# Kernel tuning notes

Hardware: AMD Instinct MI355X
Metric: run time of the kernel (lower is better)

The kernel has to match this reference:

```python
import jax, jax.numpy as jnp
import numpy as np

E, T, D, H = 8, 16384, 2048, 1024  # experts, routed tokens, hidden_size, moe_intermediate_size


def setup_inputs() -> dict:
    key = jax.random.key(0)
    k1, k2, k3, k4 = jax.random.split(key, 4)
    x = jax.random.normal(k1, (T, D), jnp.float32)
    # scale params like a trained init
    w1 = jax.random.normal(k2, (E, H, D), jnp.float32) * 0.02
    w2 = jax.random.normal(k3, (E, D, H), jnp.float32) * 0.02
    w3 = jax.random.normal(k4, (E, H, D), jnp.float32) * 0.02
    # uneven per-expert token counts summing exactly to T (tokens pre-sorted by expert)
    num_tokens_per_expert = jnp.array([3000, 1000, 2500, 1500, 2000, 2200, 1800, 2384], jnp.int32)
    return {"x": x, "w1": w1, "w2": w2, "w3": w3,
            "num_tokens_per_expert": num_tokens_per_expert}


def reference(x, w1, w2, w3, num_tokens_per_expert):
    # Grouped (ragged) GEMM expert FFN: for tokens of expert e,
    #   out = (gelu_tanh(x @ w1[e].T) * (x @ w3[e].T)) @ w2[e].T
    counts = num_tokens_per_expert.astype(jnp.int32)
    wt = lambda w: jnp.swapaxes(w, -1, -2)  # [E, in, out]
    h = jax.nn.gelu(jax.lax.ragged_dot(x, wt(w1), counts), approximate=True)  # [T, H]
    h = h * jax.lax.ragged_dot(x, wt(w3), counts)                             # [T, H]
    out = jax.lax.ragged_dot(h, wt(w2), counts)                               # [T, D]
    return out
```

## Files before the change

kernel.cpp:

```cpp
#include <hip/hip_runtime.h>
#include <hip/hip_bf16.h>
#include <math.h>

constexpr int T_ = 16384;
constexpr int D_ = 2048;
constexpr int H_ = 1024;
constexpr int E_ = 8;

constexpr int BM = 128, BK = 64;
constexpr int MT128 = T_ / 128 + E_;
constexpr int NT16  = 16;
constexpr int NGEMM = MT128 * NT16;

typedef __bf16 bf16x8 __attribute__((ext_vector_type(8)));
typedef float  f32x4  __attribute__((ext_vector_type(4)));

__device__ __forceinline__ int imin(int a, int b) { return a < b ? a : b; }

__device__ __forceinline__ bf16x8 cvt8(const float* p) {
    float4 u = *reinterpret_cast<const float4*>(p);
    float4 v = *reinterpret_cast<const float4*>(p + 4);
    bf16x8 r;
    r[0] = (__bf16)u.x; r[1] = (__bf16)u.y; r[2] = (__bf16)u.z; r[3] = (__bf16)u.w;
    r[4] = (__bf16)v.x; r[5] = (__bf16)v.y; r[6] = (__bf16)v.z; r[7] = (__bf16)v.w;
    return r;
}

__device__ __forceinline__ bf16x8 ld_lds8(const char* lds, int row, int kbyte) {
    int byte = row * 128 + (kbyte ^ ((row & 7) << 4));
    return *reinterpret_cast<const bf16x8*>(lds + byte);
}

template<int K_>
__device__ __forceinline__ void stage_glds(char* lds, const __bf16* __restrict__ src,
                                           int valid, int tid) {
    int wave = tid >> 6, l = tid & 63;
#pragma unroll
    for (int i = 0; i < 4; ++i) {
        int chunk = wave * 4 + i;
        int row = chunk * 8 + (l >> 3);
        int rc = imin(row, valid - 1);
        int colb = ((l & 7) * 16) ^ ((row & 7) << 4);
        const char* gp = reinterpret_cast<const char*>(src)
                       + (size_t)rc * (K_ * 2) + colb;
        __builtin_amdgcn_global_load_lds(
            (const __attribute__((address_space(1))) void*)gp,
            (__attribute__((address_space(3))) void*)(lds + chunk * 1024), 16, 0, 0);
    }
}

__device__ __forceinline__ bool find_expert(const int* __restrict__ counts, int mt,
                                            int& e, int& row0, int& valid) {
    int macc = 0, start = 0;
    e = -1;
    for (int i = 0; i < E_; ++i) {
        int c = counts[i];
        int t = (c + BM - 1) >> 7;
        if (e < 0 && mt < macc + t) {
            int lm = mt - macc;
            e = i; row0 = start + lm * BM; valid = imin(BM, c - lm * BM);
        }
        macc += t; start += c;
    }
    return e >= 0;
}

template<int K_, bool FUSE>
__global__ __launch_bounds__(256, 4) void gemm128(
        const __bf16* __restrict__ A, const __bf16* __restrict__ Bw,
        const int* __restrict__ counts,
        __bf16* __restrict__ hout, float* __restrict__ fout,
        const float* __restrict__ cvt_src, __bf16* __restrict__ cvt_dst,
        int cvt_n8, int nGemm) {
    if ((int)blockIdx.x >= nGemm) {
        int nb = (int)gridDim.x - nGemm;
        int i = ((int)blockIdx.x - nGemm) * 256 + (int)threadIdx.x;
        int stride = nb * 256;
        for (; i < cvt_n8; i += stride)
            *reinterpret_cast<bf16x8*>(cvt_dst + (size_t)i * 8) = cvt8(cvt_src + (size_t)i * 8);
        return;
    }
    __shared__ alignas(16) char sA[128 * 128];
    __shared__ alignas(16) char sB[128 * 128];

    int tid = threadIdx.x;
    int f = (int)blockIdx.x;
    int swz = (f & 7) * (NGEMM / 8) + (f >> 3);
    int nt = swz % NT16, mt = swz / NT16;

    int e, row0, valid;
    if (!find_expert(counts, mt, e, row0, valid)) return;

    int wid = tid >> 6, lane = tid & 63;
    int wr = wid >> 1, wc = wid & 1;
    int frow = lane & 15, fkb = (lane >> 4) * 16;

    const __bf16* Ab = A  + (size_t)row0 * K_;
    const __bf16* Bb = Bw + (size_t)e * 2048 * K_ + (size_t)(nt * 128) * K_;

    f32x4 acc[4][4] = {};

    for (int k0 = 0; k0 < K_; k0 += BK) {
        stage_glds<K_>(sA, Ab + k0, valid, tid);
        stage_glds<K_>(sB, Bb + k0, 128, tid);
        __syncthreads();
#pragma unroll
        for (int kk = 0; kk < BK; kk += 32) {
            int kb = kk * 2 + fkb;
            bf16x8 a[4], b[4];
#pragma unroll
            for (int m = 0; m < 4; ++m) a[m] = ld_lds8(sA, wr * 64 + m * 16 + frow, kb);
#pragma unroll
            for (int n = 0; n < 4; ++n) b[n] = ld_lds8(sB, wc * 64 + n * 16 + frow, kb);
#pragma unroll
            for (int m = 0; m < 4; ++m)
#pragma unroll
                for (int n = 0; n < 4; ++n)
                    acc[m][n] = __builtin_amdgcn_mfma_f32_16x16x32_bf16(a[m], b[n], acc[m][n], 0, 0, 0);
        }
        __syncthreads();
    }

    int q = lane >> 4;
#pragma unroll
    for (int m = 0; m < 4; ++m)
#pragma unroll
        for (int j = 0; j < 4; ++j) {
            int lrow = wr * 64 + m * 16 + q * 4 + j;
            if (lrow < valid) {
                size_t rg = (size_t)(row0 + lrow);
                if (FUSE) {
#pragma unroll
                    for (int p = 0; p < 2; ++p) {
                        float c1 = acc[m][2 * p][j], c3 = acc[m][2 * p + 1][j];
                        float inner = 0.7978845608028654f * (c1 + 0.044715f * c1 * c1 * c1);
                        float g = 0.5f * c1 * (1.0f + tanhf(inner));
                        int col = nt * 64 + wc * 32 + p * 16 + frow;
                        hout[rg * H_ + col] = (__bf16)(g * c3);
                    }
                } else {
#pragma unroll
                    for (int n = 0; n < 4; ++n) {
                        int col = nt * 128 + wc * 64 + n * 16 + frow;
                        fout[rg * D_ + col] = acc[m][n][j];
                    }
                }
            }
        }
}

__global__ __launch_bounds__(256) void prep(const float* __restrict__ x,
                                            __bf16* __restrict__ xb,
                                            const float* __restrict__ w1,
                                            const float* __restrict__ w3,
                                            __bf16* __restrict__ wb) {
    int bid = blockIdx.x;
    if (bid < 2048) {
        int n8 = T_ * D_ / 8;
        int i = bid * 256 + threadIdx.x, stride = 2048 * 256;
        for (; i < n8; i += stride)
            *reinterpret_cast<bf16x8*>(xb + (size_t)i * 8) = cvt8(x + (size_t)i * 8);
    } else {
        int R = (bid - 2048) & 2047, e = (bid - 2048) >> 11;
        int g = R >> 5, r5 = R & 31;
        const float* src = (r5 < 16 ? w1 : w3)
                         + ((size_t)e * H_ + g * 16 + (r5 & 15)) * D_;
        __bf16* dst = wb + ((size_t)e * 2048 + R) * D_;
        int d = threadIdx.x * 8;
        *reinterpret_cast<bf16x8*>(dst + d) = cvt8(src + d);
    }
}

extern "C" void kernel_launch(void* const* d_in, const int* in_sizes, int n_in,
                              void* d_out, int out_size, void* d_ws, size_t ws_size,
                              hipStream_t stream) {
    const float* x      = (const float*)d_in[0];
    const float* w1     = (const float*)d_in[1];
    const float* w2     = (const float*)d_in[2];
    const float* w3     = (const float*)d_in[3];
    const int*   counts = (const int*)d_in[4];
    float* out = (float*)d_out;

    const size_t XB  = (size_t)T_ * D_ * 2;
    const size_t HB  = (size_t)T_ * H_ * 2;
    const size_t WIB = (size_t)E_ * 2 * H_ * D_ * 2;

    char* ws = (char*)d_ws;
    __bf16* xb   = (__bf16*)(ws);
    __bf16* hbuf = (__bf16*)(ws + XB);
    __bf16* wb   = (__bf16*)(ws + XB + HB);
    __bf16* w2b  = (__bf16*)(ws + XB + HB + WIB);
    (void)ws_size;

    prep<<<2048 + E_ * 2048, 256, 0, stream>>>(x, xb, w1, w3, wb);

    gemm128<D_, true ><<<NGEMM + 512, 256, 0, stream>>>(
        xb, wb, counts, hbuf, nullptr, w2, w2b, E_ * D_ * H_ / 8, NGEMM);

    gemm128<H_, false><<<NGEMM, 256, 0, stream>>>(
        hbuf, w2b, counts, nullptr, out, nullptr, nullptr, 0, NGEMM);
}
```

Measured before the change: 328.7 us.

## Double-buffer LDS tiles with async global_load_lds prefetch and MFMA priority

Turns the single-buffered K loop into a double-buffered pipeline. The next K tile is issued via global_load_lds into the alternate LDS buffer before computing the current one, with explicit vmcnt waits and raw s_barriers in place of __syncthreads. It also raises wave priority around the MFMA block and lowers launch bounds to 2 blocks per CU, since LDS use per block doubles to 64KB. The aim is to hide global load latency behind matrix math, at the cost of lower occupancy.

```diff
diff --git a/kernel.cpp b/kernel.cpp
--- a/kernel.cpp
+++ b/kernel.cpp
@@ -16,6 +16,9 @@
 typedef float  f32x4  __attribute__((ext_vector_type(4)));
 
 __device__ __forceinline__ int imin(int a, int b) { return a < b ? a : b; }
+
+#define SCHED0 __builtin_amdgcn_sched_barrier(0)
+#define BARX do { SCHED0; __builtin_amdgcn_s_barrier(); SCHED0; } while (0)
 
 __device__ __forceinline__ bf16x8 cvt8(const float* p) {
     float4 u = *reinterpret_cast<const float4*>(p);
@@ -66,7 +69,7 @@
 }
 
 template<int K_, bool FUSE>
-__global__ __launch_bounds__(256, 4) void gemm128(
+__global__ __launch_bounds__(256, 2) void gemm128db(
         const __bf16* __restrict__ A, const __bf16* __restrict__ Bw,
         const int* __restrict__ counts,
         __bf16* __restrict__ hout, float* __restrict__ fout,
@@ -80,8 +83,9 @@
             *reinterpret_cast<bf16x8*>(cvt_dst + (size_t)i * 8) = cvt8(cvt_src + (size_t)i * 8);
         return;
     }
-    __shared__ alignas(16) char sA[128 * 128];
-    __shared__ alignas(16) char sB[128 * 128];
+    constexpr int NT = K_ / BK;
+    __shared__ alignas(16) char sA[2][128 * 128];
+    __shared__ alignas(16) char sB[2][128 * 128];
 
     int tid = threadIdx.x;
     int f = (int)blockIdx.x;
@@ -100,25 +104,39 @@
 
     f32x4 acc[4][4] = {};
 
-    for (int k0 = 0; k0 < K_; k0 += BK) {
-        stage_glds<K_>(sA, Ab + k0, valid, tid);
-        stage_glds<K_>(sB, Bb + k0, 128, tid);
-        __syncthreads();
+    stage_glds<K_>(sA[0], Ab, valid, tid);
+    stage_glds<K_>(sB[0], Bb, 128, tid);
+
+    for (int t = 0; t < NT; ++t) {
+        int c = t & 1, nc = c ^ 1;
+        if (t + 1 < NT) {
+            stage_glds<K_>(sA[nc], Ab + (t + 1) * BK, valid, tid);
+            stage_glds<K_>(sB[nc], Bb + (t + 1) * BK, 128, tid);
+            asm volatile("s_waitcnt vmcnt(8)" ::: "memory");
+        } else {
+            asm volatile("s_waitcnt vmcnt(0)" ::: "memory");
+        }
+        SCHED0;
+        BARX;
 #pragma unroll
         for (int kk = 0; kk < BK; kk += 32) {
             int kb = kk * 2 + fkb;
             bf16x8 a[4], b[4];
 #pragma unroll
-            for (int m = 0; m < 4; ++m) a[m] = ld_lds8(sA, wr * 64 + m * 16 + frow, kb);
-#pragma unroll
-            for (int n = 0; n < 4; ++n) b[n] = ld_lds8(sB, wc * 64 + n * 16 + frow, kb);
+            for (int m = 0; m < 4; ++m) a[m] = ld_lds8(sA[c], wr * 64 + m * 16 + frow, kb);
+#pragma unroll
+            for (int n = 0; n < 4; ++n) b[n] = ld_lds8(sB[c], wc * 64 + n * 16 + frow, kb);
+            asm volatile("s_waitcnt lgkmcnt(0)" ::: "memory");
+            SCHED0;
+            __builtin_amdgcn_s_setprio(1);
 #pragma unroll
             for (int m = 0; m < 4; ++m)
 #pragma unroll
                 for (int n = 0; n < 4; ++n)
                     acc[m][n] = __builtin_amdgcn_mfma_f32_16x16x32_bf16(a[m], b[n], acc[m][n], 0, 0, 0);
-        }
-        __syncthreads();
+            __builtin_amdgcn_s_setprio(0);
+        }
+        BARX;
     }
 
     int q = lane >> 4;
@@ -194,9 +212,9 @@
 
     prep<<<2048 + E_ * 2048, 256, 0, stream>>>(x, xb, w1, w3, wb);
 
-    gemm128<D_, true ><<<NGEMM + 512, 256, 0, stream>>>(
+    gemm128db<D_, true ><<<NGEMM + 512, 256, 0, stream>>>(
         xb, wb, counts, hbuf, nullptr, w2, w2b, E_ * D_ * H_ / 8, NGEMM);
 
-    gemm128<H_, false><<<NGEMM, 256, 0, stream>>>(
+    gemm128db<H_, false><<<NGEMM, 256, 0, stream>>>(
         hbuf, w2b, counts, nullptr, out, nullptr, nullptr, 0, NGEMM);
 }
```

Result: slower. 430.3 us (+30.9%).

## Fuse both expert GEMMs into one persistent kernel with per-tile dependency counters

Applied to the files above, without the earlier changes.

Replaces the two GEMM launches with a single persistent kernel of 768 blocks. Each block walks a task list: w2 conversion tasks first, then the up-projection tiles, then the down-projection tiles. Down-projection tiles spin on atomic counters until w2 is converted and all 16 up-projection tiles of their row block are done. This removes the kernel boundary and lets the second GEMM overlap the tail of the first, at the cost of spin-wait overhead, an extra memset, and deadlock risk if not every block is resident at once. The path is only taken when the workspace has room for the counters; otherwise the old two-launch path runs.

```diff
diff --git a/kernel.cpp b/kernel.cpp
--- a/kernel.cpp
+++ b/kernel.cpp
@@ -11,6 +11,10 @@
 constexpr int MT128 = T_ / 128 + E_;
 constexpr int NT16  = 16;
 constexpr int NGEMM = MT128 * NT16;
+
+constexpr int NW2   = 512;
+constexpr int NTASK = NW2 + 2 * NGEMM;
+constexpr int PERS  = 768;
 
 typedef __bf16 bf16x8 __attribute__((ext_vector_type(8)));
 typedef float  f32x4  __attribute__((ext_vector_type(4)));
@@ -63,6 +67,120 @@
         macc += t; start += c;
     }
     return e >= 0;
+}
+
+template<int K_, bool FUSE>
+__device__ __forceinline__ void gemm_body(char* sA, char* sB, int tid,
+        int nt, int e, int row0, int valid,
+        const __bf16* __restrict__ A, const __bf16* __restrict__ Bw,
+        __bf16* __restrict__ hout, float* __restrict__ fout) {
+    int wid = tid >> 6, lane = tid & 63;
+    int wr = wid >> 1, wc = wid & 1;
+    int frow = lane & 15, fkb = (lane >> 4) * 16;
+
+    const __bf16* Ab = A  + (size_t)row0 * K_;
+    const __bf16* Bb = Bw + (size_t)e * 2048 * K_ + (size_t)(nt * 128) * K_;
+
+    f32x4 acc[4][4] = {};
+
+    for (int k0 = 0; k0 < K_; k0 += BK) {
+        stage_glds<K_>(sA, Ab + k0, valid, tid);
+        stage_glds<K_>(sB, Bb + k0, 128, tid);
+        __syncthreads();
+#pragma unroll
+        for (int kk = 0; kk < BK; kk += 32) {
+            int kb = kk * 2 + fkb;
+            bf16x8 a[4], b[4];
+#pragma unroll
+            for (int m = 0; m < 4; ++m) a[m] = ld_lds8(sA, wr * 64 + m * 16 + frow, kb);
+#pragma unroll
+            for (int n = 0; n < 4; ++n) b[n] = ld_lds8(sB, wc * 64 + n * 16 + frow, kb);
+#pragma unroll
+            for (int m = 0; m < 4; ++m)
+#pragma unroll
+                for (int n = 0; n < 4; ++n)
+                    acc[m][n] = __builtin_amdgcn_mfma_f32_16x16x32_bf16(a[m], b[n], acc[m][n], 0, 0, 0);
+        }
+        __syncthreads();
+    }
+
+    int q = lane >> 4;
+#pragma unroll
+    for (int m = 0; m < 4; ++m)
+#pragma unroll
+        for (int j = 0; j < 4; ++j) {
+            int lrow = wr * 64 + m * 16 + q * 4 + j;
+            if (lrow < valid) {
+                size_t rg = (size_t)(row0 + lrow);
+                if (FUSE) {
+#pragma unroll
+                    for (int p = 0; p < 2; ++p) {
+                        float c1 = acc[m][2 * p][j], c3 = acc[m][2 * p + 1][j];
+                        float inner = 0.7978845608028654f * (c1 + 0.044715f * c1 * c1 * c1);
+                        float g = 0.5f * c1 * (1.0f + tanhf(inner));
+                        int col = nt * 64 + wc * 32 + p * 16 + frow;
+                        hout[rg * H_ + col] = (__bf16)(g * c3);
+                    }
+                } else {
+#pragma unroll
+                    for (int n = 0; n < 4; ++n) {
+                        int col = nt * 128 + wc * 64 + n * 16 + frow;
+                        fout[rg * D_ + col] = acc[m][n][j];
+                    }
+                }
+            }
+        }
+}
+
+__global__ __launch_bounds__(256, 4) void ffn_fused(
+        const __bf16* __restrict__ xb, const __bf16* __restrict__ wb,
+        __bf16* __restrict__ w2b, const float* __restrict__ w2,
+        const int* __restrict__ counts,
+        __bf16* __restrict__ hbuf, float* __restrict__ out,
+        int* __restrict__ ctr) {
+    __shared__ alignas(16) char sA[128 * 128];
+    __shared__ alignas(16) char sB[128 * 128];
+    int tid = threadIdx.x;
+
+    for (int task = (int)blockIdx.x; task < NTASK; task += PERS) {
+        if (task < NW2) {
+            int n8 = E_ * D_ * H_ / 8;
+            for (int i = task * 256 + tid; i < n8; i += NW2 * 256)
+                *reinterpret_cast<bf16x8*>(w2b + (size_t)i * 8) = cvt8(w2 + (size_t)i * 8);
+            __threadfence();
+            __syncthreads();
+            if (tid == 0) atomicAdd(&ctr[1], 1);
+            __syncthreads();
+        } else if (task < NW2 + NGEMM) {
+            int f = task - NW2;
+            int swz = (f & 7) * (NGEMM / 8) + (f >> 3);
+            int nt = swz % NT16, mt = swz / NT16;
+            int e, row0, valid;
+            bool ok = find_expert(counts, mt, e, row0, valid);
+            if (ok) {
+                gemm_body<D_, true>(sA, sB, tid, nt, e, row0, valid, xb, wb, hbuf, nullptr);
+                __threadfence();
+            }
+            __syncthreads();
+            if (ok && tid == 0) atomicAdd(&ctr[2 + mt], 1);
+            __syncthreads();
+        } else {
+            int f = task - NW2 - NGEMM;
+            int swz = (f & 7) * (NGEMM / 8) + (f >> 3);
+            int nt = swz % NT16, mt = swz / NT16;
+            int e, row0, valid;
+            if (find_expert(counts, mt, e, row0, valid)) {
+                if (tid == 0) {
+                    while (atomicAdd(&ctr[1], 0) < NW2) __builtin_amdgcn_s_sleep(32);
+                    while (atomicAdd(&ctr[2 + mt], 0) < NT16) __builtin_amdgcn_s_sleep(32);
+                    __threadfence();
+                }
+                __syncthreads();
+                gemm_body<H_, false>(sA, sB, tid, nt, e, row0, valid, hbuf, w2b, nullptr, out);
+                __syncthreads();
+            }
+        }
+    }
 }
 
 template<int K_, bool FUSE>
@@ -82,71 +200,13 @@
     }
     __shared__ alignas(16) char sA[128 * 128];
     __shared__ alignas(16) char sB[128 * 128];
-
     int tid = threadIdx.x;
     int f = (int)blockIdx.x;
     int swz = (f & 7) * (NGEMM / 8) + (f >> 3);
     int nt = swz % NT16, mt = swz / NT16;
-
     int e, row0, valid;
     if (!find_expert(counts, mt, e, row0, valid)) return;
-
-    int wid = tid >> 6, lane = tid & 63;
-    int wr = wid >> 1, wc = wid & 1;
-    int frow = lane & 15, fkb = (lane >> 4) * 16;
-
-    const __bf16* Ab = A  + (size_t)row0 * K_;
-    const __bf16* Bb = Bw + (size_t)e * 2048 * K_ + (size_t)(nt * 128) * K_;
-
-    f32x4 acc[4][4] = {};
-
-    for (int k0 = 0; k0 < K_; k0 += BK) {
-        stage_glds<K_>(sA, Ab + k0, valid, tid);
-        stage_glds<K_>(sB, Bb + k0, 128, tid);
-        __syncthreads();
-#pragma unroll
-        for (int kk = 0; kk < BK; kk += 32) {
-            int kb = kk * 2 + fkb;
-            bf16x8 a[4], b[4];
-#pragma unroll
-            for (int m = 0; m < 4; ++m) a[m] = ld_lds8(sA, wr * 64 + m * 16 + frow, kb);
-#pragma unroll
-            for (int n = 0; n < 4; ++n) b[n] = ld_lds8(sB, wc * 64 + n * 16 + frow, kb);
-#pragma unroll
-            for (int m = 0; m < 4; ++m)
-#pragma unroll
-                for (int n = 0; n < 4; ++n)
-                    acc[m][n] = __builtin_amdgcn_mfma_f32_16x16x32_bf16(a[m], b[n], acc[m][n], 0, 0, 0);
-        }
-        __syncthreads();
-    }
-
-    int q = lane >> 4;
-#pragma unroll
-    for (int m = 0; m < 4; ++m)
-#pragma unroll
-        for (int j = 0; j < 4; ++j) {
-            int lrow = wr * 64 + m * 16 + q * 4 + j;
-            if (lrow < valid) {
-                size_t rg = (size_t)(row0 + lrow);
-                if (FUSE) {
-#pragma unroll
-                    for (int p = 0; p < 2; ++p) {
-                        float c1 = acc[m][2 * p][j], c3 = acc[m][2 * p + 1][j];
-                        float inner = 0.7978845608028654f * (c1 + 0.044715f * c1 * c1 * c1);
-                        float g = 0.5f * c1 * (1.0f + tanhf(inner));
-                        int col = nt * 64 + wc * 32 + p * 16 + frow;
-                        hout[rg * H_ + col] = (__bf16)(g * c3);
-                    }
-                } else {
-#pragma unroll
-                    for (int n = 0; n < 4; ++n) {
-                        int col = nt * 128 + wc * 64 + n * 16 + frow;
-                        fout[rg * D_ + col] = acc[m][n][j];
-                    }
-                }
-            }
-        }
+    gemm_body<K_, FUSE>(sA, sB, tid, nt, e, row0, valid, A, Bw, hout, fout);
 }
 
 __global__ __launch_bounds__(256) void prep(const float* __restrict__ x,
@@ -184,19 +244,25 @@
     const size_t XB  = (size_t)T_ * D_ * 2;
     const size_t HB  = (size_t)T_ * H_ * 2;
     const size_t WIB = (size_t)E_ * 2 * H_ * D_ * 2;
+    const size_t W2B = (size_t)E_ * D_ * H_ * 2;
+    const size_t CTRO = XB + HB + WIB + W2B;
 
     char* ws = (char*)d_ws;
     __bf16* xb   = (__bf16*)(ws);
     __bf16* hbuf = (__bf16*)(ws + XB);
     __bf16* wb   = (__bf16*)(ws + XB + HB);
     __bf16* w2b  = (__bf16*)(ws + XB + HB + WIB);
-    (void)ws_size;
+    int* ctr     = (int*)(ws + CTRO);
 
     prep<<<2048 + E_ * 2048, 256, 0, stream>>>(x, xb, w1, w3, wb);
 
-    gemm128<D_, true ><<<NGEMM + 512, 256, 0, stream>>>(
-        xb, wb, counts, hbuf, nullptr, w2, w2b, E_ * D_ * H_ / 8, NGEMM);
-
-    gemm128<H_, false><<<NGEMM, 256, 0, stream>>>(
-        hbuf, w2b, counts, nullptr, out, nullptr, nullptr, 0, NGEMM);
-}
+    if (ws_size >= CTRO + 1024) {
+        hipMemsetAsync(ctr, 0, 1024, stream);
+        ffn_fused<<<PERS, 256, 0, stream>>>(xb, wb, w2b, w2, counts, hbuf, out, ctr);
+    } else {
+        gemm128<D_, true ><<<NGEMM + 512, 256, 0, stream>>>(
+            xb, wb, counts, hbuf, nullptr, w2, w2b, E_ * D_ * H_ / 8, NGEMM);
+        gemm128<H_, false><<<NGEMM, 256, 0, stream>>>(
+            hbuf, w2b, counts, nullptr, out, nullptr, nullptr, 0, NGEMM);
+    }
+}
```

New measurement: 799.0 us. +143.1%, slower.
